# Optimization experiments

Hardware: AMD Instinct MI355X
Metric: run time of the kernel (lower is better)

Reference implementation:

```python
import jax, jax.numpy as jnp
import numpy as np

ENC_IN = 512
D_MODEL = 1024
EMB_DIM = 32
IN_DIM = D_MODEL + EMB_DIM  # 1056
BATCH = 64


def setup_inputs() -> dict:
    key = jax.random.key(0)
    ks = jax.random.split(key, 12)
    s = 0.02
    return {
        "x": jax.random.normal(ks[0], (BATCH, ENC_IN, D_MODEL), dtype=jnp.float32),
        "emb": jax.random.normal(ks[1], (ENC_IN, EMB_DIM), dtype=jnp.float32) * s,
        # weights stored [in, out] (transposed vs torch Linear, same math)
        "w1": jax.random.normal(ks[2], (IN_DIM, IN_DIM), dtype=jnp.float32) * s,
        "b1": jnp.zeros((IN_DIM,), dtype=jnp.float32),
        "wq": jax.random.normal(ks[3], (IN_DIM, IN_DIM), dtype=jnp.float32) * s,
        "bq": jnp.zeros((IN_DIM,), dtype=jnp.float32),
        "wk": jax.random.normal(ks[4], (IN_DIM, IN_DIM), dtype=jnp.float32) * s,
        "bk": jnp.zeros((IN_DIM,), dtype=jnp.float32),
        "wv": jax.random.normal(ks[5], (IN_DIM, IN_DIM), dtype=jnp.float32) * s,
        "bv": jnp.zeros((IN_DIM,), dtype=jnp.float32),
        "w2": jax.random.normal(ks[6], (IN_DIM, D_MODEL), dtype=jnp.float32) * s,
        "b2": jnp.zeros((D_MODEL,), dtype=jnp.float32),
    }


def reference(x, emb, w1, b1, wq, bq, wk, bk, wv, bv, w2, b2):
    B = x.shape[0]
    # variable embedding: same for every batch element -> broadcast concat
    e = jnp.broadcast_to(emb[None, :, :], (B, ENC_IN, EMB_DIM))
    h = jnp.concatenate([x, e], axis=2)                      # [B, S, IN_DIM]
    h = jax.nn.leaky_relu(h @ w1 + b1, negative_slope=0.2)   # l1
    # hand-rolled self-attention: no scaling, softmax over last dim
    q = h @ wq + bq
    k = h @ wk + bk
    v = h @ wv + bv
    energy = jnp.einsum("bsd,btd->bst", q, k)                # [B, S, S]
    attn = jax.nn.softmax(energy, axis=-1)
    out = jnp.einsum("bst,btd->bsd", attn, v)                # [B, S, IN_DIM]
    return out @ w2 + b2                                     # [B, S, D_MODEL]
```

## Files before the change

### kernel.cpp

```cpp
#include <hip/hip_runtime.h>
#include <hip/hip_bf16.h>
#include <cstdint>

typedef __hip_bfloat16 bf16;
typedef __attribute__((ext_vector_type(8))) short short8;
typedef __attribute__((ext_vector_type(4))) float f32x4;

__device__ __forceinline__ void gload16(const bf16* g, bf16* l) {
    __builtin_amdgcn_global_load_lds(
        (__attribute__((address_space(1))) void*)g,
        (__attribute__((address_space(3))) void*)l, 16, 0, 0);
}
#define VMC(n) asm volatile("s_waitcnt vmcnt(" #n ")" ::: "memory")
__device__ __forceinline__ void bar() {
    asm volatile("" ::: "memory");
    __builtin_amdgcn_s_barrier();
    asm volatile("" ::: "memory");
}

__device__ __forceinline__ void stage_half(const bf16* __restrict__ G, int ld,
                                           int row0, int k0, bf16* lregion,
                                           int w, int lrow, int lslot)
{
    const bf16* s0 = G + (long long)(row0 + w * 8 + lrow) * ld + (k0 + lslot * 8);
    gload16(s0, lregion + (w * 64) * 8);
    gload16(s0 + (long long)64 * ld, lregion + (512 + w * 64) * 8);
}

#define LOAD_AI(dst, i_, mh, P) do { \
    _Pragma("unroll") for (int ks_ = 0; ks_ < 2; ++ks_) \
      dst[i_][ks_] = *(const short8*)((P) + ((mh) * 64 + (i_) * 16 + l15) * 64 \
                                         + (((ks_ * 4 + lq) ^ l7) * 8)); } while (0)
#define LOAD_B(nh, dst) do { _Pragma("unroll") for (int j_ = 0; j_ < 2; ++j_) { \
    _Pragma("unroll") for (int ks_ = 0; ks_ < 2; ++ks_) \
      dst[j_][ks_] = *(const short8*)(pb + (bhr + (nh) * 32 + j_ * 16 + l15) * 64 \
                                         + (((ks_ * 4 + lq) ^ l7) * 8)); } } while (0)
#define DO_Q(mh, nh, AF, BF) do { \
    __builtin_amdgcn_s_setprio(1); \
    _Pragma("unroll") for (int i_ = 0; i_ < 4; ++i_) \
      _Pragma("unroll") for (int j_ = 0; j_ < 2; ++j_) \
        _Pragma("unroll") for (int ks_ = 0; ks_ < 2; ++ks_) \
          acc[mh][nh][i_][j_] = __builtin_amdgcn_mfma_f32_16x16x32_bf16( \
              AF[i_][ks_], BF[j_][ks_], acc[mh][nh][i_][j_], 0, 0, 0); \
    __builtin_amdgcn_s_setprio(0); \
} while (0)

template<int OUT_BF16, int ACT, int BIASMODE, int ROUTE>
__device__ __forceinline__ void gemm_core(
    bf16* ldsb,
    const bf16* __restrict__ Abase, const bf16* __restrict__ Bbase,
    void* __restrict__ Cbase, const float* __restrict__ bias,
    int K, int lda, int ldb, int ldc, int nwrite,
    long long sA, long long sB, long long sC, long long segStride,
    int bx, int by, int bz)
{
    const int tid = threadIdx.x;
    const int wid = tid >> 6, lane = tid & 63;
    const int wm = wid >> 2, wn = wid & 3;
    const int l15 = lane & 15, l7 = lane & 7, lq = lane >> 4;
    const int lrow = lane >> 3, lslot = l7 ^ lrow;
    const int bhr = (wn & 1) * 64;

    const bf16* A = Abase + (long long)bz * sA;
    const bf16* B = Bbase + (long long)bz * sB;
    const int brow = by * 256, bcol = bx * 256;

    f32x4 acc[2][2][4][2] = {};
    short8 aFe[4][2], aFo[4][2], bF0[2][2], bF1[2][2];

    const int nt = K >> 6;

    stage_half(B, ldb, bcol,       0,  ldsb + 2 * 8192, wid, lrow, lslot);
    stage_half(B, ldb, bcol + 128, 0,  ldsb + 3 * 8192, wid, lrow, lslot);
    stage_half(A, lda, brow,       0,  ldsb,            wid, lrow, lslot);
    stage_half(A, lda, brow + 128, 0,  ldsb + 1 * 8192, wid, lrow, lslot);
    stage_half(B, ldb, bcol,       64, ldsb + 6 * 8192, wid, lrow, lslot);
    stage_half(B, ldb, bcol + 128, 64, ldsb + 7 * 8192, wid, lrow, lslot);
    VMC(4);
    bar();

    for (int t = 0; t < nt; ++t) {
        const int b = t & 1;
        const bf16* pa = ldsb + (b * 4 + wm) * 8192;
        const bf16* pb = ldsb + (b * 4 + 2 + (wn >> 1)) * 8192;
        bf16* oA = ldsb + ((b ^ 1) * 4) * 8192;
        bf16* cB = ldsb + (b * 4 + 2) * 8192;
        const int t1 = (t + 1 == nt) ? 0 : t + 1;
        const int t2 = (t + 2 >= nt) ? t + 2 - nt : t + 2;
        const int k1 = t1 << 6, k2 = t2 << 6;

        LOAD_B(0, bF0);
        LOAD_AI(aFe, 0, 0, pa); LOAD_AI(aFe, 1, 0, pa);
        LOAD_AI(aFe, 2, 0, pa); LOAD_AI(aFe, 3, 0, pa);
        LOAD_B(1, bF1);
        stage_half(A, lda, brow, k1, oA, wid, lrow, lslot);
        bar();
        DO_Q(0, 0, aFe, bF0);
        bar();

        LOAD_AI(aFo, 0, 1, pa); LOAD_AI(aFo, 1, 1, pa);
        stage_half(A, lda, brow + 128, k1, oA + 8192, wid, lrow, lslot);
        bar();
        DO_Q(0, 1, aFe, bF1);
        bar();

        LOAD_AI(aFo, 2, 1, pa); LOAD_AI(aFo, 3, 1, pa);
        stage_half(B, ldb, bcol, k2, cB, wid, lrow, lslot);
        bar();
        DO_Q(1, 1, aFo, bF1);
        bar();

        stage_half(B, ldb, bcol + 128, k2, cB + 8192, wid, lrow, lslot);
        bar();
        DO_Q(1, 0, aFo, bF0);
        VMC(4);
        bar();
    }
    VMC(0);

    const long long cofs0 = (long long)bz * sC;
    #pragma unroll
    for (int mh = 0; mh < 2; ++mh)
      #pragma unroll
      for (int nh = 0; nh < 2; ++nh)
        #pragma unroll
        for (int i = 0; i < 4; ++i)
          #pragma unroll
          for (int j = 0; j < 2; ++j) {
              const int gc = bcol + wn * 64 + nh * 32 + j * 16 + l15;
              const bool wr = gc < nwrite;
              const int row0 = brow + wm * 128 + mh * 64 + i * 16 + lq * 4;
              if (wr) {
                  float bvv = 0.0f;
                  if (BIASMODE == 1) bvv = bias[gc];
                  if (BIASMODE == 3) bvv = bias[(long long)bz * 512 + gc];
                  if (ROUTE == 2 && gc < 1024) {
                      const int b_ = row0 >> 9, s_ = row0 & 511;
                      bf16 t4[4];
                      #pragma unroll
                      for (int rr = 0; rr < 4; ++rr) {
                          float vv = acc[mh][nh][i][j][rr] + bvv;
                          t4[rr] = (bf16)vv;
                      }
                      *(ushort4*)&((bf16*)Cbase)[((long long)b_ * 1024 + gc) * 512 + s_]
                          = *(ushort4*)t4;
                  } else {
                      long long base; int lc, ld;
                      if (ROUTE == 2) { base = segStride; lc = gc - 1024; ld = 1088; }
                      else { base = cofs0; lc = gc; ld = ldc; }
                      #pragma unroll
                      for (int rr = 0; rr < 4; ++rr) {
                          float vv = acc[mh][nh][i][j][rr] + bvv;
                          if (ACT) vv = vv > 0.0f ? vv : 0.2f * vv;
                          const long long cidx = base + (long long)(row0 + rr) * ld + lc;
                          if (OUT_BF16) ((bf16*)Cbase)[cidx] = (bf16)vv;
                          else          ((float*)Cbase)[cidx] = vv;
                      }
                  }
              }
          }
}

template<int OUT_BF16, int ACT, int BIASMODE, int ROUTE>
__global__ __launch_bounds__(512, 2)
void gemm256(const bf16* __restrict__ Abase, const bf16* __restrict__ Bbase,
             void* __restrict__ Cbase, const float* __restrict__ bias,
             int K, int lda, int ldb, int ldc, int nwrite,
             long long sA, long long sB, long long sC, long long segStride)
{
    __shared__ bf16 lds[8][8192];
    const int gx = gridDim.x, gy = gridDim.y;
    const int nwg = gx * gy * gridDim.z;
    const int lin = blockIdx.x + gx * (blockIdx.y + gy * blockIdx.z);
    const int qch = nwg >> 3, rch = nwg & 7;
    const int xcd = lin & 7, pos = lin >> 3;
    const int nl = (xcd < rch ? xcd * (qch + 1)
                              : rch * (qch + 1) + (xcd - rch) * qch) + pos;
    const int bz = nl / (gx * gy);
    const int rem = nl - bz * (gx * gy);
    const int by = rem / gx;
    const int bx = rem - by * gx;
    gemm_core<OUT_BF16, ACT, BIASMODE, ROUTE>(
        &lds[0][0], Abase, Bbase, Cbase, bias, K, lda, ldb, ldc, nwrite,
        sA, sB, sC, segStride, bx, by, bz);
}

__global__ __launch_bounds__(512, 2)
void mega0_kernel(const float* __restrict__ x, const float* __restrict__ emb,
                  const bf16* __restrict__ wkC, const bf16* __restrict__ wqC,
                  const bf16* __restrict__ w2T, const bf16* __restrict__ wvC,
                  bf16* __restrict__ Bqv, bf16* __restrict__ hcat,
                  const float* __restrict__ wk, const float* __restrict__ bq,
                  float* __restrict__ uvec,
                  const float* __restrict__ b1, float* __restrict__ b1p,
                  const float* __restrict__ bv, const float* __restrict__ w2,
                  const float* __restrict__ b2, float* __restrict__ b2p2)
{
    __shared__ bf16 lds[8][8192];
    const int lin = blockIdx.x;
    const int tid = threadIdx.x;
    if (lin < 25) {
        gemm_core<1, 0, 0, 0>(&lds[0][0], wkC, wqC, Bqv + 1024LL * 1088, nullptr,
                              1088, 1088, 1088, 1088, 1088, 0, 0, 0, 0,
                              lin % 5, lin / 5, 0);
    } else if (lin < 45) {
        const int l = lin - 25;
        gemm_core<1, 0, 0, 0>(&lds[0][0], w2T, wvC, Bqv, nullptr,
                              1088, 1088, 1088, 1088, 1088, 0, 0, 0, 0,
                              l % 5, l / 5, 0);
    } else if (lin < 16429) {
        const int m = (lin - 45) * 2 + (tid >> 8);
        const int t = tid & 255;
        const int s = m & 511;
        const float* xr = x + (long long)m * 1024;
        bf16* orow = hcat + (long long)m * 1088;
        for (int g = t; g < 272; g += 256) {
            const int c = g * 4;
            float4 v;
            if (c < 1024)      v = *(const float4*)&xr[c];
            else if (c < 1056) v = *(const float4*)&emb[s * 32 + (c - 1024)];
            else               v = make_float4(0.f, 0.f, 0.f, 0.f);
            bf16 tt[4] = { (bf16)v.x, (bf16)v.y, (bf16)v.z, (bf16)v.w };
            *(ushort4*)&orow[c] = *(ushort4*)tt;
        }
    } else if (lin < 16565) {
        const int wid = tid >> 6, lane = tid & 63;
        const int e = (lin - 16429) * 8 + wid;
        if (e < 1088) {
            float s = 0.0f;
            if (e < 1056) {
                for (int d = lane; d < 1056; d += 64)
                    s += wk[(long long)e * 1056 + d] * bq[d];
            }
            #pragma unroll
            for (int sh = 32; sh > 0; sh >>= 1) s += __shfl_xor(s, sh);
            if (lane == 0) uvec[e] = s;
        }
    } else if (lin < 16568) {
        const int i = (lin - 16565) * 512 + tid;
        if (i < 1088) b1p[i] = (i < 1056) ? b1[i] : 0.0f;
    } else {
        const int l = lin - 16568;
        const int nn = l * 64 + (tid & 63), oq = tid >> 6;
        float s = 0.0f;
        for (int o = oq; o < 1056; o += 8)
            s += bv[o] * w2[(long long)o * 1024 + nn];
        float* red = (float*)&lds[0][0];
        red[tid] = s;
        __syncthreads();
        if (tid < 64) {
            float t2 = b2[l * 64 + tid];
            #pragma unroll
            for (int q = 0; q < 8; ++q) t2 += red[q * 64 + tid];
            b2p2[l * 64 + tid] = t2;
        }
    }
}

__global__ void wprep_kernel(const float* __restrict__ w1, const float* __restrict__ wv,
                             const float* __restrict__ w2, const float* __restrict__ wq,
                             const float* __restrict__ wk,
                             bf16* __restrict__ w1T, bf16* __restrict__ wvC,
                             bf16* __restrict__ w2T, bf16* __restrict__ wqC,
                             bf16* __restrict__ wkC)
{
    const int z = blockIdx.z;
    const int tx = threadIdx.x, ty = threadIdx.y;
    if (z == 1 || z >= 3) {
        const float* src = (z == 1) ? wv : (z == 3) ? wq : wk;
        bf16* dst = (z == 1) ? wvC : (z == 3) ? wqC : wkC;
        const int r = blockIdx.y * 32 + ty, c = blockIdx.x * 32 + tx;
        if (r < 1280 && c < 1088) {
            float v = (r < 1056 && c < 1056) ? src[(long long)r * 1056 + c] : 0.0f;
            dst[(long long)r * 1088 + c] = (bf16)v;
        }
        return;
    }
    const float* src; bf16* dst; int NIN, NP, srcld;
    if (z == 0) { src = w1; dst = w1T; NIN = 1056; NP = 1280; srcld = 1056; }
    else        { src = w2; dst = w2T; NIN = 1024; NP = 1024; srcld = 1024; }
    const int KIN = 1056, KP = 1088;
    const int k0 = blockIdx.x * 32, n0 = blockIdx.y * 32;
    if (n0 >= NP) return;
    __shared__ float t[32][33];
    const int kk = k0 + ty, nn = n0 + tx;
    t[ty][tx] = (kk < KIN && nn < NIN) ? src[(long long)kk * srcld + nn] : 0.0f;
    __syncthreads();
    const int ko = k0 + tx, no = n0 + ty;
    if (no < NP && ko < KP)
        dst[(long long)no * KP + ko] = (bf16)t[tx][ty];
}

__global__ __launch_bounds__(256)
void cvec_kernel(const bf16* __restrict__ h, const float* __restrict__ u,
                 float* __restrict__ c)
{
    __shared__ float sred[256];
    __shared__ int nz;
    const int tid = threadIdx.x;
    float su = 0.0f;
    for (int i = tid; i < 1088; i += 256) su += fabsf(u[i]);
    sred[tid] = su;
    __syncthreads();
    if (tid < 128) sred[tid] += sred[tid + 128];
    __syncthreads();
    if (tid < 64) sred[tid] += sred[tid + 64];
    __syncthreads();
    if (tid == 0) {
        float t = 0.0f;
        for (int i = 0; i < 64; ++i) t += sred[i];
        nz = (t != 0.0f);
    }
    __syncthreads();
    const int wid = tid >> 6, lane = tid & 63;
    const long long row = (long long)blockIdx.x * 4 + wid;
    if (!nz) {
        if (lane == 0) c[row] = 0.0f;
        return;
    }
    const bf16* hr = h + row * 1088;
    float s = 0.0f;
    #pragma unroll
    for (int j = 0; j < 17; ++j)
        s += (float)hr[j * 64 + lane] * u[j * 64 + lane];
    #pragma unroll
    for (int sh = 32; sh > 0; sh >>= 1) s += __shfl_xor(s, sh);
    if (lane == 0) c[row] = s;
}

__global__ __launch_bounds__(256)
void softmax_kernel(const float* __restrict__ e, bf16* __restrict__ p)
{
    const int wid = threadIdx.x >> 6, lane = threadIdx.x & 63;
    const long long row = (long long)blockIdx.x * 4 + wid;
    const float* er = e + row * 512;
    float v[8];
    float mx = -3.0e38f;
    #pragma unroll
    for (int j = 0; j < 8; ++j) { v[j] = er[j * 64 + lane]; mx = fmaxf(mx, v[j]); }
    #pragma unroll
    for (int s = 32; s > 0; s >>= 1) mx = fmaxf(mx, __shfl_xor(mx, s));
    float sum = 0.0f;
    #pragma unroll
    for (int j = 0; j < 8; ++j) { v[j] = __expf(v[j] - mx); sum += v[j]; }
    #pragma unroll
    for (int s = 32; s > 0; s >>= 1) sum += __shfl_xor(sum, s);
    const float inv = 1.0f / sum;
    bf16* pr = p + row * 512;
    #pragma unroll
    for (int j = 0; j < 8; ++j) pr[j * 64 + lane] = (bf16)(v[j] * inv);
}

extern "C" void kernel_launch(void* const* d_in, const int* in_sizes, int n_in,
                              void* d_out, int out_size, void* d_ws, size_t ws_size,
                              hipStream_t stream)
{
    const float* x   = (const float*)d_in[0];
    const float* emb = (const float*)d_in[1];
    const float* w1  = (const float*)d_in[2];
    const float* b1  = (const float*)d_in[3];
    const float* wq  = (const float*)d_in[4];
    const float* bq  = (const float*)d_in[5];
    const float* wk  = (const float*)d_in[6];
    const float* wv  = (const float*)d_in[8];
    const float* bv  = (const float*)d_in[9];
    const float* w2  = (const float*)d_in[10];
    const float* b2  = (const float*)d_in[11];
    float* out = (float*)d_out;

    const long long Mrows = 32768;
    const int KR = 1088;

    char* ws = (char*)d_ws;
    size_t off = 0;
    auto alloc = [&](size_t bytes) -> char* {
        char* p = ws + off;
        off += (bytes + 255) & ~(size_t)255;
        return p;
    };
    char* R1   = alloc((size_t)Mrows * KR * 2);
    char* Rh   = alloc((size_t)Mrows * KR * 2);
    char* Rq   = alloc((size_t)Mrows * KR * 2);
    bf16* v2T  = (bf16*)alloc((size_t)64 * 1024 * 512 * 2);
    bf16* w1T  = (bf16*)alloc((size_t)1280 * KR * 2);
    bf16* Bqv  = (bf16*)alloc((size_t)2304 * KR * 2);
    bf16* w2T  = (bf16*)alloc((size_t)1024 * KR * 2);
    bf16* wqC  = (bf16*)alloc((size_t)1280 * KR * 2);
    bf16* wkC  = (bf16*)alloc((size_t)1280 * KR * 2);
    bf16* wvC  = (bf16*)alloc((size_t)1280 * KR * 2);
    float* b1p  = (float*)alloc((size_t)1088 * 4);
    float* b2p2 = (float*)alloc((size_t)1024 * 4);
    float* uvec = (float*)alloc((size_t)1088 * 4);
    float* cvec = (float*)alloc((size_t)Mrows * 4);

    bf16*  hcat   = (bf16*)R1;
    float* energy = (float*)R1;
    bf16*  h      = (bf16*)Rh;
    bf16*  qbuf   = (bf16*)Rq;
    bf16*  attn   = (bf16*)Rq;

    wprep_kernel<<<dim3(34, 40, 5), dim3(32, 32), 0, stream>>>(
        w1, wv, w2, wq, wk, w1T, wvC, w2T, wqC, wkC);
    mega0_kernel<<<16584, 512, 0, stream>>>(
        x, emb, wkC, wqC, w2T, wvC, Bqv, hcat,
        wk, bq, uvec, b1, b1p, bv, w2, b2, b2p2);
    gemm256<1, 1, 1, 0><<<dim3(5, 128, 1), 512, 0, stream>>>(
        hcat, w1T, h, b1p, KR, KR, KR, KR, KR, 0, 0, 0, 0);
    cvec_kernel<<<8192, 256, 0, stream>>>(h, uvec, cvec);
    gemm256<1, 0, 0, 2><<<dim3(9, 128, 1), 512, 0, stream>>>(
        h, Bqv, v2T, nullptr, KR, KR, KR, 0, 2112, 0, 0, 0,
        (long long)(qbuf - v2T));
    gemm256<0, 0, 3, 0><<<dim3(2, 2, 64), 512, 0, stream>>>(
        qbuf, h, energy, cvec, KR, KR, KR, 512, 512,
        512LL * KR, 512LL * KR, 512LL * 512, 0);
    softmax_kernel<<<8192, 256, 0, stream>>>(energy, attn);
    gemm256<0, 0, 1, 0><<<dim3(4, 2, 64), 512, 0, stream>>>(
        attn, v2T, out, b2p2, 512, 512, 512, 1024, 1024,
        512LL * 512, 1024LL * 512, 512LL * 1024, 0);
}
```

Baseline: 567.3 us.

## Replace double-buffered LDS pipeline with single buffer and fewer barriers

The GEMM main loop moves from a double-buffered LDS ring (8 slabs, with A and B prefetched one and two tiles ahead) to a single buffer of 4 slabs. Each iteration reads all fragments into registers, waits on LDS reads, then issues the next tile's global-to-LDS loads while the second half of the MFMAs runs. This halves LDS use per block, which may allow more blocks per CU, and cuts the per-iteration barriers from eight to two. The cost is that global-load latency is hidden only behind half an iteration's compute, with a full vmcnt(0) wait before every iteration.

```diff
diff --git a/kernel.cpp b/kernel.cpp
--- a/kernel.cpp
+++ b/kernel.cpp
@@ -12,6 +12,7 @@
         (__attribute__((address_space(3))) void*)l, 16, 0, 0);
 }
 #define VMC(n) asm volatile("s_waitcnt vmcnt(" #n ")" ::: "memory")
+#define LGKM0 asm volatile("s_waitcnt lgkmcnt(0)" ::: "memory")
 __device__ __forceinline__ void bar() {
     asm volatile("" ::: "memory");
     __builtin_amdgcn_s_barrier();
@@ -70,53 +71,44 @@
 
     const int nt = K >> 6;
 
-    stage_half(B, ldb, bcol,       0,  ldsb + 2 * 8192, wid, lrow, lslot);
-    stage_half(B, ldb, bcol + 128, 0,  ldsb + 3 * 8192, wid, lrow, lslot);
-    stage_half(A, lda, brow,       0,  ldsb,            wid, lrow, lslot);
-    stage_half(A, lda, brow + 128, 0,  ldsb + 1 * 8192, wid, lrow, lslot);
-    stage_half(B, ldb, bcol,       64, ldsb + 6 * 8192, wid, lrow, lslot);
-    stage_half(B, ldb, bcol + 128, 64, ldsb + 7 * 8192, wid, lrow, lslot);
-    VMC(4);
+    stage_half(B, ldb, bcol,       0, ldsb + 2 * 8192, wid, lrow, lslot);
+    stage_half(B, ldb, bcol + 128, 0, ldsb + 3 * 8192, wid, lrow, lslot);
+    stage_half(A, lda, brow,       0, ldsb,            wid, lrow, lslot);
+    stage_half(A, lda, brow + 128, 0, ldsb + 8192,     wid, lrow, lslot);
+    VMC(0);
     bar();
 
+    const bf16* pa = ldsb + wm * 8192;
+    const bf16* pb = ldsb + 16384 + (wn >> 1) * 8192;
+
     for (int t = 0; t < nt; ++t) {
-        const int b = t & 1;
-        const bf16* pa = ldsb + (b * 4 + wm) * 8192;
-        const bf16* pb = ldsb + (b * 4 + 2 + (wn >> 1)) * 8192;
-        bf16* oA = ldsb + ((b ^ 1) * 4) * 8192;
-        bf16* cB = ldsb + (b * 4 + 2) * 8192;
         const int t1 = (t + 1 == nt) ? 0 : t + 1;
-        const int t2 = (t + 2 >= nt) ? t + 2 - nt : t + 2;
-        const int k1 = t1 << 6, k2 = t2 << 6;
+        const int k1 = t1 << 6;
 
         LOAD_B(0, bF0);
         LOAD_AI(aFe, 0, 0, pa); LOAD_AI(aFe, 1, 0, pa);
         LOAD_AI(aFe, 2, 0, pa); LOAD_AI(aFe, 3, 0, pa);
         LOAD_B(1, bF1);
-        stage_half(A, lda, brow, k1, oA, wid, lrow, lslot);
+        LOAD_AI(aFo, 0, 1, pa); LOAD_AI(aFo, 1, 1, pa);
+        LOAD_AI(aFo, 2, 1, pa); LOAD_AI(aFo, 3, 1, pa);
+
+        DO_Q(0, 0, aFe, bF0);
+        DO_Q(0, 1, aFe, bF1);
+
+        LGKM0;
         bar();
-        DO_Q(0, 0, aFe, bF0);
-        bar();
-
-        LOAD_AI(aFo, 0, 1, pa); LOAD_AI(aFo, 1, 1, pa);
-        stage_half(A, lda, brow + 128, k1, oA + 8192, wid, lrow, lslot);
-        bar();
-        DO_Q(0, 1, aFe, bF1);
-        bar();
-
-        LOAD_AI(aFo, 2, 1, pa); LOAD_AI(aFo, 3, 1, pa);
-        stage_half(B, ldb, bcol, k2, cB, wid, lrow, lslot);
-        bar();
+
+        stage_half(B, ldb, bcol,       k1, ldsb + 2 * 8192, wid, lrow, lslot);
+        stage_half(B, ldb, bcol + 128, k1, ldsb + 3 * 8192, wid, lrow, lslot);
+        stage_half(A, lda, brow,       k1, ldsb,            wid, lrow, lslot);
+        stage_half(A, lda, brow + 128, k1, ldsb + 8192,     wid, lrow, lslot);
+
         DO_Q(1, 1, aFo, bF1);
-        bar();
-
-        stage_half(B, ldb, bcol + 128, k2, cB + 8192, wid, lrow, lslot);
-        bar();
         DO_Q(1, 0, aFo, bF0);
-        VMC(4);
+
+        VMC(0);
         bar();
     }
-    VMC(0);
 
     const long long cofs0 = (long long)bz * sC;
     #pragma unroll
@@ -168,7 +160,7 @@
              int K, int lda, int ldb, int ldc, int nwrite,
              long long sA, long long sB, long long sC, long long segStride)
 {
-    __shared__ bf16 lds[8][8192];
+    __shared__ bf16 lds[4][8192];
     const int gx = gridDim.x, gy = gridDim.y;
     const int nwg = gx * gy * gridDim.z;
     const int lin = blockIdx.x + gx * (blockIdx.y + gy * blockIdx.z);
@@ -196,7 +188,7 @@
                   const float* __restrict__ bv, const float* __restrict__ w2,
                   const float* __restrict__ b2, float* __restrict__ b2p2)
 {
-    __shared__ bf16 lds[8][8192];
+    __shared__ bf16 lds[4][8192];
     const int lin = blockIdx.x;
     const int tid = threadIdx.x;
     if (lin < 25) {
```

Result: slower. 627.9 us (+10.7%).
